# Performance work log

Hardware: AMD Instinct MI355X
Metric: run time of the kernel (lower is better)

## Reference

```python
import jax, jax.numpy as jnp
import numpy as np

C = 256
NUM_HEADS = 8
FFN_HIDDEN = C * 2  # ffn_expand=2
EPS = 1e-5


def setup_inputs() -> dict:
    key = jax.random.key(0)
    ks = jax.random.split(key, 12)
    B, H, W = 16, 64, 64
    s = 0.02
    return {
        "optical": jax.random.normal(ks[0], (B, C, H, W), jnp.float32),
        "sar": jax.random.normal(ks[1], (B, C, H, W), jnp.float32),
        "g_opt": jnp.ones((C,), jnp.float32),
        "b_opt": jnp.zeros((C,), jnp.float32),
        "g_sar": jnp.ones((C,), jnp.float32),
        "b_sar": jnp.zeros((C,), jnp.float32),
        "Wq": jax.random.normal(ks[2], (C, C), jnp.float32) * s,
        "Wk": jax.random.normal(ks[3], (C, C), jnp.float32) * s,
        "Wv": jax.random.normal(ks[4], (C, C), jnp.float32) * s,
        "Wo": jax.random.normal(ks[5], (C, C), jnp.float32) * s,
        "g_ffn": jnp.ones((C,), jnp.float32),
        "b_ffn": jnp.zeros((C,), jnp.float32),
        "W1": jax.random.normal(ks[6], (2 * FFN_HIDDEN, C), jnp.float32) * s,
        "b1": jnp.zeros((2 * FFN_HIDDEN,), jnp.float32),
        "W2": jax.random.normal(ks[7], (C, FFN_HIDDEN), jnp.float32) * s,
        "b2": jnp.zeros((C,), jnp.float32),
    }


def _ln(x, g, b):
    # LayerNorm over channel axis of (B, C, H, W), biased variance, eps=1e-5
    mu = jnp.mean(x, axis=1, keepdims=True)
    var = jnp.mean(jnp.square(x - mu), axis=1, keepdims=True)
    xn = (x - mu) * jax.lax.rsqrt(var + EPS)
    return xn * g[None, :, None, None] + b[None, :, None, None]


def _proj(x, Wmat):
    # 1x1 conv == channel matmul
    return jnp.einsum('oc,bchw->bohw', Wmat, x)


def reference(optical, sar, g_opt, b_opt, g_sar, b_sar, Wq, Wk, Wv, Wo,
              g_ffn, b_ffn, W1, b1, W2, b2):
    B, Cc, H, W = optical.shape
    hc = Cc // NUM_HEADS
    L = H * W
    scale = hc ** -0.5

    opt_n = _ln(optical, g_opt, b_opt)
    sar_n = _ln(sar, g_sar, b_sar)

    # channel (transposed) attention: contraction over spatial L
    q = _proj(opt_n, Wq).reshape(B, NUM_HEADS, hc, L)
    k = _proj(sar_n, Wk).reshape(B, NUM_HEADS, hc, L)
    v = _proj(sar_n, Wv).reshape(B, NUM_HEADS, hc, L)
    A = jax.nn.softmax(jnp.einsum('bhcl,bhdl->bhcd', q, k) * scale, axis=-1)
    attn = jnp.einsum('bhcd,bhdl->bhcl', A, v).reshape(B, Cc, H, W)
    x = optical + _proj(attn, Wo)

    # SimpleGate FFN
    h = _ln(x, g_ffn, b_ffn)
    h = _proj(h, W1) + b1[None, :, None, None]
    h1, h2 = jnp.split(h, 2, axis=1)
    h = _proj(h1 * h2, W2) + b2[None, :, None, None]
    return x + h
```

## Files before the change

### kernel.cpp

```cpp
#include <hip/hip_runtime.h>
#include <hip/hip_bf16.h>

typedef __bf16 bf16;
typedef __attribute__((ext_vector_type(8))) __bf16 bf16x8;
typedef __attribute__((ext_vector_type(4))) __bf16 bf16x4;
typedef __attribute__((ext_vector_type(4))) float f32x4;
typedef __attribute__((ext_vector_type(16))) float f32x16;

#define LSP 4096
#define CCH 256

__device__ __forceinline__ void gl2lds16(const bf16* g, bf16* l) {
  __builtin_amdgcn_global_load_lds(
      (const __attribute__((address_space(1))) unsigned int*)g,
      (__attribute__((address_space(3))) unsigned int*)l, 16, 0, 0);
}

__device__ __forceinline__ f32x4 mfma16(bf16x8 a, bf16x8 b, f32x4 c) {
  return __builtin_amdgcn_mfma_f32_16x16x32_bf16(a, b, c, 0, 0, 0);
}
__device__ __forceinline__ f32x16 mfma32(bf16x8 a, bf16x8 b, f32x16 c) {
  return __builtin_amdgcn_mfma_f32_32x32x16_bf16(a, b, c, 0, 0, 0);
}

__global__ __launch_bounds__(256) void cvt_w_kernel(
    const float* __restrict__ wq, const float* __restrict__ wk,
    const float* __restrict__ wv, const float* __restrict__ wo,
    const float* __restrict__ w1, const float* __restrict__ w2,
    const float* __restrict__ gff, bf16* __restrict__ out) {
  int e = blockIdx.x * 256 + threadIdx.x;
  if (e < 65536)        { out[e] = (bf16)wq[e]; }
  else if (e < 131072)  { out[e] = (bf16)wk[e - 65536]; }
  else if (e < 196608)  {
    int e2 = e - 131072;
    int och = e2 >> 8, cin = e2 & 255;
    out[131072 + cin * 256 + och] = (bf16)wv[e2];
  }
  else if (e < 262144)  { out[e] = (bf16)wo[e - 196608]; }
  else if (e < 524288)  {
    int e2 = e - 262144;
    int m = e2 >> 8, k = e2 & 255;
    int mp = (m < 512) ? (2 * m) : (2 * (m - 512) + 1);
    out[262144 + mp * 256 + k] = (bf16)(w1[e2] * gff[k]);
  }
  else                  { out[e] = (bf16)w2[e - 524288]; }
}

__global__ __launch_bounds__(256) void w1vec_kernel(
    const float* __restrict__ w1, const float* __restrict__ b1,
    const float* __restrict__ gff, const float* __restrict__ bff,
    float* __restrict__ cvec) {
  int m = blockIdx.x * 256 + threadIdx.x;
  const float* row = w1 + (size_t)m * 256;
  float sb = 0.f, sg = 0.f;
  #pragma unroll 8
  for (int c = 0; c < 256; c += 4) {
    f32x4 w = *(const f32x4*)&row[c];
    f32x4 g = *(const f32x4*)&gff[c];
    f32x4 bb = *(const f32x4*)&bff[c];
    #pragma unroll
    for (int j = 0; j < 4; ++j) { sb += w[j] * bb[j]; sg += w[j] * g[j]; }
  }
  if (m < 512) {
    cvec[m] = sb + b1[m];
    cvec[512 + m] = sg;
  } else {
    cvec[512 + m] = sb + b1[m];
    cvec[1024 + m] = sg;
  }
}

template <int DUAL>
__global__ __launch_bounds__(256) void ln_tile_kernel(
    const float* __restrict__ x, const float* __restrict__ gam,
    const float* __restrict__ bet, bf16* __restrict__ out_cl,
    bf16* __restrict__ out_lc) {
  const int l0 = blockIdx.x * 64;
  const int b  = blockIdx.y;
  const int tid = threadIdx.x;
  __shared__ bf16 Tt[256 * 64];
  __shared__ float red[2][16][64];
  __shared__ float mu_s[64], rs_s[64];

  const float* px = x + (size_t)b * CCH * LSP + l0;
  const int colq = (tid & 15) * 4;
  f32x4 s = {0.f, 0.f, 0.f, 0.f}, q = {0.f, 0.f, 0.f, 0.f};
  #pragma unroll
  for (int it = 0; it < 16; ++it) {
    int c = it * 16 + (tid >> 4);
    f32x4 v = *(const f32x4*)&px[(size_t)c * LSP + colq];
    s += v;
    q += v * v;
    bf16x4 h;
    #pragma unroll
    for (int j = 0; j < 4; ++j) h[j] = (bf16)v[j];
    int colp = colq ^ (((c >> 3) & 7) << 3);
    *(bf16x4*)&Tt[c * 64 + colp] = h;
  }
  #pragma unroll
  for (int j = 0; j < 4; ++j) {
    red[0][tid >> 4][colq + j] = s[j];
    red[1][tid >> 4][colq + j] = q[j];
  }
  __syncthreads();
  if (tid < 64) {
    float S = 0.f, Q = 0.f;
    #pragma unroll
    for (int k = 0; k < 16; ++k) { S += red[0][k][tid]; Q += red[1][k][tid]; }
    float m = S * (1.f / 256.f);
    mu_s[tid] = m;
    rs_s[tid] = rsqrtf(Q * (1.f / 256.f) - m * m + 1e-5f);
  }
  __syncthreads();

  #pragma unroll
  for (int it = 0; it < 8; ++it) {
    int ch = it * 256 + tid;
    int c = ch >> 3, col8 = (ch & 7) * 8;
    int colp = col8 ^ (((c >> 3) & 7) << 3);
    bf16x8 h = *(const bf16x8*)&Tt[c * 64 + colp];
    f32x4 m0 = *(const f32x4*)&mu_s[col8];
    f32x4 m1 = *(const f32x4*)&mu_s[col8 + 4];
    f32x4 r0 = *(const f32x4*)&rs_s[col8];
    f32x4 r1 = *(const f32x4*)&rs_s[col8 + 4];
    float g = gam[c], be = bet[c];
    bf16x8 o;
    #pragma unroll
    for (int j = 0; j < 4; ++j) {
      o[j]     = (bf16)(((float)h[j] - m0[j]) * r0[j] * g + be);
      o[4 + j] = (bf16)(((float)h[4 + j] - m1[j]) * r1[j] * g + be);
    }
    *(bf16x8*)&out_cl[((size_t)b * CCH + c) * LSP + l0 + col8] = o;
  }

  if constexpr (DUAL) {
    #pragma unroll
    for (int it = 0; it < 8; ++it) {
      int ch = it * 256 + tid;
      int l = ch >> 5, cch = ch & 31;
      int c0 = cch * 8;
      int lp = l ^ ((cch & 7) << 3);
      float mu = mu_s[l], rs = rs_s[l];
      f32x4 g0 = *(const f32x4*)&gam[c0];
      f32x4 g1 = *(const f32x4*)&gam[c0 + 4];
      f32x4 b0 = *(const f32x4*)&bet[c0];
      f32x4 b1 = *(const f32x4*)&bet[c0 + 4];
      bf16x8 o;
      #pragma unroll
      for (int j = 0; j < 4; ++j) {
        float h0 = (float)Tt[(c0 + j) * 64 + lp];
        float h1 = (float)Tt[(c0 + 4 + j) * 64 + lp];
        o[j]     = (bf16)((h0 - mu) * rs * g0[j] + b0[j]);
        o[4 + j] = (bf16)((h1 - mu) * rs * g1[j] + b1[j]);
      }
      *(bf16x8*)&out_lc[((size_t)b * LSP + l0 + l) * CCH + c0] = o;
    }
  }
}

__global__ __launch_bounds__(256) void gram_kernel(
    const bf16* __restrict__ sar_cl, const bf16* __restrict__ opt_cl,
    float* __restrict__ part) {
  const int tile = blockIdx.x, chunk = blockIdx.y, b = blockIdx.z;
  const int tid = threadIdx.x, lane = tid & 63, w = tid >> 6;
  const int j0 = (tile >> 1) * 128 + (w >> 1) * 64;
  const int i0 = (tile & 1) * 128 + (w & 1) * 64;
  const int l0 = chunk * 1024;
  const bf16* sj = sar_cl + ((size_t)b * CCH + j0 + (lane & 31)) * LSP + l0;
  const bf16* oi = opt_cl + ((size_t)b * CCH + i0 + (lane & 31)) * LSP + l0;
  f32x16 acc[2][2];
  #pragma unroll
  for (int mt = 0; mt < 2; ++mt)
    #pragma unroll
    for (int nt = 0; nt < 2; ++nt)
      #pragma unroll
      for (int r = 0; r < 16; ++r) acc[mt][nt][r] = 0.f;
  #pragma unroll 4
  for (int ks = 0; ks < 64; ++ks) {
    int lofs = ks * 16 + (lane >> 5) * 8;
    bf16x8 a0 = *(const bf16x8*)&sj[lofs];
    bf16x8 a1 = *(const bf16x8*)&sj[32 * LSP + lofs];
    bf16x8 b0 = *(const bf16x8*)&oi[lofs];
    bf16x8 b1 = *(const bf16x8*)&oi[32 * LSP + lofs];
    acc[0][0] = mfma32(a0, b0, acc[0][0]);
    acc[0][1] = mfma32(a0, b1, acc[0][1]);
    acc[1][0] = mfma32(a1, b0, acc[1][0]);
    acc[1][1] = mfma32(a1, b1, acc[1][1]);
  }
  float* op = part + ((size_t)chunk * 16 + b) * 65536;
  #pragma unroll
  for (int mt = 0; mt < 2; ++mt)
    #pragma unroll
    for (int nt = 0; nt < 2; ++nt)
      #pragma unroll
      for (int r = 0; r < 16; ++r) {
        int row = j0 + mt * 32 + (r & 3) + 8 * (r >> 2) + 4 * (lane >> 5);
        int col = i0 + nt * 32 + (lane & 31);
        op[(size_t)row * 256 + col] = acc[mt][nt][r];
      }
}

__global__ __launch_bounds__(256) void greduce_kernel(
    const float* __restrict__ part, bf16* __restrict__ G2) {
  size_t e = ((size_t)blockIdx.x * 256 + threadIdx.x) * 8;
  float a[8];
  #pragma unroll
  for (int i = 0; i < 8; ++i) a[i] = 0.f;
  #pragma unroll
  for (int ch = 0; ch < 4; ++ch) {
    f32x4 p0 = *(const f32x4*)&part[ch * 1048576ull + e];
    f32x4 p1 = *(const f32x4*)&part[ch * 1048576ull + e + 4];
    #pragma unroll
    for (int i = 0; i < 4; ++i) { a[i] += p0[i]; a[4 + i] += p1[i]; }
  }
  bf16x8 o;
  #pragma unroll
  for (int i = 0; i < 8; ++i) o[i] = (bf16)a[i];
  *(bf16x8*)&G2[e] = o;
}

__global__ __launch_bounds__(256) void fold2_kernel(
    const bf16* __restrict__ G2, const bf16* __restrict__ Wq,
    const bf16* __restrict__ Wk, const bf16* __restrict__ WvT,
    bf16* __restrict__ UT) {
  const int bh = blockIdx.x;
  const int b = bh >> 3, h = bh & 7;
  const int tid = threadIdx.x, lane = tid & 63, w = tid >> 6;
  __shared__ bf16 M1[32 * 256];
  __shared__ float Sp[4][1024];
  __shared__ float S[1024];
  __shared__ bf16 P[1024];

  const bf16* gq = Wq + (size_t)(h * 32) * 256;
  const bf16* g2b = G2 + (size_t)b * 65536;
  #pragma unroll
  for (int mt = 0; mt < 2; ++mt)
    #pragma unroll
    for (int nt = 0; nt < 4; ++nt) {
      f32x4 acc = {0.f, 0.f, 0.f, 0.f};
      #pragma unroll
      for (int ks = 0; ks < 8; ++ks) {
        bf16x8 a = *(const bf16x8*)&gq[(size_t)(mt * 16 + (lane & 15)) * 256 +
                                       ks * 32 + (lane >> 4) * 8];
        bf16x8 bb = *(const bf16x8*)&g2b[
            (size_t)(w * 64 + nt * 16 + (lane & 15)) * 256 + ks * 32 +
            (lane >> 4) * 8];
        acc = mfma16(a, bb, acc);
      }
      #pragma unroll
      for (int r = 0; r < 4; ++r)
        M1[(mt * 16 + (lane >> 4) * 4 + r) * 256 + w * 64 + nt * 16 +
           (lane & 15)] = (bf16)acc[r];
    }
  __syncthreads();

  const bf16* gk = Wk + (size_t)(h * 32) * 256;
  #pragma unroll
  for (int mt = 0; mt < 2; ++mt)
    #pragma unroll
    for (int dt = 0; dt < 2; ++dt) {
      f32x4 acc = {0.f, 0.f, 0.f, 0.f};
      #pragma unroll
      for (int kk = 0; kk < 2; ++kk) {
        bf16x8 a = *(const bf16x8*)&M1[(mt * 16 + (lane & 15)) * 256 + w * 64 +
                                       kk * 32 + (lane >> 4) * 8];
        bf16x8 bb = *(const bf16x8*)&gk[(size_t)(dt * 16 + (lane & 15)) * 256 +
                                        w * 64 + kk * 32 + (lane >> 4) * 8];
        acc = mfma16(a, bb, acc);
      }
      #pragma unroll
      for (int r = 0; r < 4; ++r)
        Sp[w][(mt * 16 + (lane >> 4) * 4 + r) * 32 + dt * 16 + (lane & 15)] =
            acc[r];
    }
  __syncthreads();
  #pragma unroll
  for (int i = 0; i < 4; ++i) {
    int e = tid + 256 * i;
    S[e] = (Sp[0][e] + Sp[1][e] + Sp[2][e] + Sp[3][e]) * 0.17677669529663687f;
  }
  __syncthreads();
  if (tid < 32) {
    float m = -1e30f;
    #pragma unroll
    for (int d = 0; d < 32; ++d) m = fmaxf(m, S[tid * 32 + d]);
    float sum = 0.f;
    float ex[32];
    #pragma unroll
    for (int d = 0; d < 32; ++d) {
      ex[d] = __expf(S[tid * 32 + d] - m);
      sum += ex[d];
    }
    float inv = 1.f / sum;
    #pragma unroll
    for (int d = 0; d < 32; ++d) P[tid * 32 + d] = (bf16)(ex[d] * inv);
  }
  __syncthreads();

  bf16x8 bfrag[2];
  #pragma unroll
  for (int ct = 0; ct < 2; ++ct)
    bfrag[ct] =
        *(const bf16x8*)&P[(ct * 16 + (lane & 15)) * 32 + (lane >> 4) * 8];
  bf16* outb = UT + (size_t)b * 65536 + h * 32;
  #pragma unroll
  for (int t = 0; t < 4; ++t) {
    int cin16 = w * 64 + t * 16;
    bf16x8 afrag = *(const bf16x8*)&WvT[(size_t)(cin16 + (lane & 15)) * 256 +
                                        h * 32 + (lane >> 4) * 8];
    #pragma unroll
    for (int ct = 0; ct < 2; ++ct) {
      f32x4 acc = {0.f, 0.f, 0.f, 0.f};
      acc = mfma16(afrag, bfrag[ct], acc);
      int c = ct * 16 + (lane & 15);
      int cinr = cin16 + (lane >> 4) * 4;
      #pragma unroll
      for (int r = 0; r < 4; ++r)
        outb[(size_t)(cinr + r) * 256 + c] = (bf16)acc[r];
    }
  }
}

__global__ __launch_bounds__(256) void wfold_kernel(
    const bf16* __restrict__ Aw, const bf16* __restrict__ Bx,
    bf16* __restrict__ outp) {
  const int tid = threadIdx.x;
  const int lane = tid & 63;
  const int wave = tid >> 6;
  const int wr = wave >> 1, wc = wave & 1;
  const int l0 = blockIdx.x * 128;
  const int m0 = blockIdx.y * 128;
  const int b  = blockIdx.z;
  constexpr int NB = 4096;
  __shared__ bf16 smem[4 * NB];
  bf16* As = smem;
  bf16* Bs = smem + 2 * NB;
  const bf16* Ag = Aw + (size_t)m0 * 256;
  const bf16* Bg = Bx + ((size_t)b * 256 + l0) * 256;
  auto stage = [&](int buf, int k0) {
    #pragma unroll
    for (int i = 0; i < 2; ++i) {
      int ch = i * 256 + tid;
      int r  = ch >> 2;
      int c8 = (ch & 3) * 8;
      gl2lds16(Ag + (size_t)r * 256 + k0 + c8, As + buf * NB + ch * 8);
      gl2lds16(Bg + (size_t)r * 256 + k0 + c8, Bs + buf * NB + ch * 8);
    }
  };
  f32x4 acc[4][4];
  #pragma unroll
  for (int mi = 0; mi < 4; ++mi)
    #pragma unroll
    for (int ni = 0; ni < 4; ++ni)
      #pragma unroll
      for (int r = 0; r < 4; ++r) acc[mi][ni][r] = 0.f;
  stage(0, 0);
  for (int kt = 0; kt < 8; ++kt) {
    __syncthreads();
    if (kt + 1 < 8) stage((kt + 1) & 1, (kt + 1) * 32);
    const bf16* Ab = As + (kt & 1) * NB;
    const bf16* Bb = Bs + (kt & 1) * NB;
    bf16x8 af[4], bfr[4];
    #pragma unroll
    for (int mi = 0; mi < 4; ++mi)
      af[mi] = *(const bf16x8*)&Ab[(wr * 64 + mi * 16 + (lane & 15)) * 32 +
                                   (lane >> 4) * 8];
    #pragma unroll
    for (int ni = 0; ni < 4; ++ni)
      bfr[ni] = *(const bf16x8*)&Bb[(wc * 64 + ni * 16 + (lane & 15)) * 32 +
                                    (lane >> 4) * 8];
    #pragma unroll
    for (int mi = 0; mi < 4; ++mi)
      #pragma unroll
      for (int ni = 0; ni < 4; ++ni)
        acc[mi][ni] = mfma16(af[mi], bfr[ni], acc[mi][ni]);
  }
  const int mq = m0 + wr * 64 + (lane >> 4) * 4;
  const int lq = l0 + wc * 64 + (lane & 15);
  #pragma unroll
  for (int mi = 0; mi < 4; ++mi)
    #pragma unroll
    for (int ni = 0; ni < 4; ++ni) {
      int l = lq + ni * 16, mb = mq + mi * 16;
      #pragma unroll
      for (int r = 0; r < 4; ++r)
        outp[((size_t)b * 256 + mb + r) * 256 + l] = (bf16)acc[mi][ni][r];
    }
}

__global__ __launch_bounds__(256) void xgemm_stats_kernel(
    const bf16* __restrict__ Wfold, const bf16* __restrict__ sar_lc,
    const float* __restrict__ optical, bf16* __restrict__ xout,
    float* __restrict__ stats) {
  const int tid = threadIdx.x, lane = tid & 63, w = tid >> 6;
  const int l0 = blockIdx.x * 64;
  const int b  = blockIdx.y;
  __shared__ __align__(16) char smem[43520];
  bf16* X = (bf16*)smem;
  float* red = (float*)(smem + 40960);

  const bf16* Ag = Wfold + (size_t)b * 65536;
  const bf16* Bg = sar_lc + ((size_t)b * LSP + l0) * CCH;

  auto stage = [&](int buf, int k0) {
    bf16* As = (bf16*)(smem + buf * 16384);
    bf16* Bs = (bf16*)(smem + 32768 + buf * 4096);
    #pragma unroll
    for (int i = 0; i < 4; ++i) {
      int ch = i * 256 + tid;
      int r = ch >> 2, c8 = (ch & 3) * 8;
      gl2lds16(Ag + (size_t)r * 256 + k0 + c8, &As[ch * 8]);
    }
    {
      int r = tid >> 2, c8 = (tid & 3) * 8;
      gl2lds16(Bg + (size_t)r * 256 + k0 + c8, &Bs[tid * 8]);
    }
  };

  f32x4 acc[4][4];
  #pragma unroll
  for (int mi = 0; mi < 4; ++mi)
    #pragma unroll
    for (int ni = 0; ni < 4; ++ni)
      #pragma unroll
      for (int r = 0; r < 4; ++r) acc[mi][ni][r] = 0.f;

  stage(0, 0);
  for (int kt = 0; kt < 8; ++kt) {
    __syncthreads();
    if (kt < 7) stage((kt + 1) & 1, (kt + 1) * 32);
    const bf16* Ab = (const bf16*)(smem + (kt & 1) * 16384);
    const bf16* Bb = (const bf16*)(smem + 32768 + (kt & 1) * 4096);
    bf16x8 af[4], bfr[4];
    #pragma unroll
    for (int mi = 0; mi < 4; ++mi)
      af[mi] = *(const bf16x8*)&Ab[(w * 64 + mi * 16 + (lane & 15)) * 32 +
                                   (lane >> 4) * 8];
    #pragma unroll
    for (int ni = 0; ni < 4; ++ni)
      bfr[ni] = *(const bf16x8*)&Bb[(ni * 16 + (lane & 15)) * 32 +
                                    (lane >> 4) * 8];
    #pragma unroll
    for (int mi = 0; mi < 4; ++mi)
      #pragma unroll
      for (int ni = 0; ni < 4; ++ni)
        acc[mi][ni] = mfma16(af[mi], bfr[ni], acc[mi][ni]);
  }
  __syncthreads();

  const int cb = w * 64 + (lane >> 4) * 4;
  const int lb = lane & 15;
  float s[4], q[4];
  #pragma unroll
  for (int ni = 0; ni < 4; ++ni) { s[ni] = 0.f; q[ni] = 0.f; }
  #pragma unroll
  for (int mi = 0; mi < 4; ++mi)
    #pragma unroll
    for (int ni = 0; ni < 4; ++ni) {
      int c = cb + mi * 16, ll = lb + ni * 16;
      bf16x4 hx;
      #pragma unroll
      for (int r = 0; r < 4; ++r) {
        float v = acc[mi][ni][r] +
                  optical[((size_t)b * CCH + c + r) * LSP + l0 + ll];
        s[ni] += v; q[ni] += v * v;
        hx[r] = (bf16)v;
      }
      *(bf16x4*)&X[ll * 260 + c] = hx;
    }
  #pragma unroll
  for (int ni = 0; ni < 4; ++ni) {
    s[ni] += __shfl_xor(s[ni], 16);
    s[ni] += __shfl_xor(s[ni], 32);
    q[ni] += __shfl_xor(q[ni], 16);
    q[ni] += __shfl_xor(q[ni], 32);
  }
  if ((lane >> 4) == 0) {
    #pragma unroll
    for (int ni = 0; ni < 4; ++ni) {
      red[(0 * 4 + w) * 64 + ni * 16 + lb] = s[ni];
      red[(4 + w) * 64 + ni * 16 + lb] = q[ni];
    }
  }
  __syncthreads();
  if (tid < 64) {
    float S4 = red[0 * 64 + tid] + red[1 * 64 + tid] + red[2 * 64 + tid] +
               red[3 * 64 + tid];
    float Q4 = red[4 * 64 + tid] + red[5 * 64 + tid] + red[6 * 64 + tid] +
               red[7 * 64 + tid];
    float m = S4 * (1.f / 256.f);
    float rs = rsqrtf(Q4 * (1.f / 256.f) - m * m + 1e-5f);
    float* st = stats + ((size_t)b * LSP + l0 + tid) * 2;
    st[0] = m;
    st[1] = rs;
  }
  __syncthreads();
  #pragma unroll
  for (int it = 0; it < 8; ++it) {
    int cid = it * 256 + tid;
    int l = cid >> 5, c0 = (cid & 31) * 8;
    bf16x8 v = *(const bf16x8*)&X[l * 260 + c0];
    *(bf16x8*)&xout[((size_t)b * LSP + l0 + l) * CCH + c0] = v;
  }
}

template <int KEL, int MODE>
__global__ __launch_bounds__(512, 2) void ffn_gemm_kernel(
    const bf16* __restrict__ Aw, const bf16* __restrict__ Bx,
    void* __restrict__ outp, const bf16* __restrict__ resb,
    const float* __restrict__ bias, const float* __restrict__ stats) {
  constexpr int LDSB = (MODE == 1) ? 135168 : 131072;
  __shared__ __align__(16) char smem_raw[LDSB];
  const int tid = threadIdx.x;
  const int lane = tid & 63;
  const int wave = tid >> 6;
  const int wr = wave >> 2;
  const int wc = wave & 3;
  const int l0 = blockIdx.x * 256;
  const int m0 = blockIdx.y * 256;
  const int b  = blockIdx.z;

  char* ldsA0 = smem_raw;
  char* ldsB0 = smem_raw + 32768;
  char* ldsA1 = smem_raw + 65536;
  char* ldsB1 = smem_raw + 98304;

  const bf16* Ag = Aw + (size_t)m0 * KEL;
  const bf16* Bg = Bx + ((size_t)b * LSP + l0) * KEL;

  auto STAGE = [&](const bf16* gsrc, char* ldst, int par, int kt) {
    #pragma unroll
    for (int i = 0; i < 2; ++i) {
      int qi = i * 512 + tid;
      int r  = ((qi >> 7) << 5) + (par << 4) + ((qi >> 3) & 15);
      int cl = (qi & 7) ^ ((qi >> 3) & 7);
      int p  = ((qi >> 7) << 8) + (par << 7) + (qi & 127);
      gl2lds16(gsrc + (size_t)r * KEL + kt * 64 + cl * 8,
               (bf16*)(ldst + p * 16));
    }
  };

  f32x4 acc[8][4];
  #pragma unroll
  for (int mi = 0; mi < 8; ++mi)
    #pragma unroll
    for (int ni = 0; ni < 4; ++ni)
      #pragma unroll
      for (int r = 0; r < 4; ++r) acc[mi][ni][r] = 0.f;

  bf16x8 af[4][2], bf[2][2];
  const int col0 = (((lane >> 4) << 4)) ^ ((lane & 7) << 4);
  const int col1 = col0 ^ 64;
  const int arow_off = (lane & 15) * 128;

#define LOAD_FRAGS(BUFA, BUFB, MP, NP)                                        \
  {                                                                           \
    const char* Ab_ = (BUFA);                                                 \
    const char* Bb_ = (BUFB);                                                 \
    _Pragma("unroll") for (int j = 0; j < 4; ++j) {                           \
      int rb = (wr * 128 + ((MP) + 2 * j) * 16) * 128 + arow_off;             \
      af[j][0] = *(const bf16x8*)(Ab_ + rb + col0);                           \
      af[j][1] = *(const bf16x8*)(Ab_ + rb + col1);                           \
    }                                                                         \
    _Pragma("unroll") for (int i = 0; i < 2; ++i) {                           \
      int rb = (wc * 64 + ((NP) + 2 * i) * 16) * 128 + arow_off;              \
      bf[i][0] = *(const bf16x8*)(Bb_ + rb + col0);                           \
      bf[i][1] = *(const bf16x8*)(Bb_ + rb + col1);                           \
    }                                                                         \
  }

#define DO_MFMA(MP, NP)                                                       \
  _Pragma("unroll") for (int j = 0; j < 4; ++j)                               \
  _Pragma("unroll") for (int i = 0; i < 2; ++i) {                             \
    acc[(MP) + 2 * j][(NP) + 2 * i] =                                         \
        mfma16(af[j][0], bf[i][0], acc[(MP) + 2 * j][(NP) + 2 * i]);          \
    acc[(MP) + 2 * j][(NP) + 2 * i] =                                         \
        mfma16(af[j][1], bf[i][1], acc[(MP) + 2 * j][(NP) + 2 * i]);          \
  }

#define PHASE(BUFA, BUFB, MP, NP, STG)                                        \
  asm volatile("s_waitcnt vmcnt(6)" ::: "memory");                            \
  __builtin_amdgcn_s_barrier();                                               \
  __builtin_amdgcn_sched_barrier(0);                                          \
  LOAD_FRAGS(BUFA, BUFB, MP, NP);                                             \
  STG;                                                                        \
  asm volatile("s_waitcnt lgkmcnt(0)" ::: "memory");                          \
  __builtin_amdgcn_sched_barrier(0);                                          \
  __builtin_amdgcn_s_setprio(1);                                              \
  DO_MFMA(MP, NP);                                                            \
  __builtin_amdgcn_s_setprio(0);

  STAGE(Ag, ldsA0, 0, 0);
  STAGE(Ag, ldsA0, 1, 0);
  STAGE(Bg, ldsB0, 0, 0);
  STAGE(Bg, ldsB0, 1, 0);
  STAGE(Ag, ldsA1, 0, 1);
  STAGE(Bg, ldsB1, 0, 1);

  constexpr int NITER = KEL / 128;
  for (int t = 0; t < NITER; ++t) {
    const int kt1 = 2 * t + 1;
    PHASE(ldsA0, ldsB0, 0, 0, STAGE(Ag, ldsA1, 1, kt1));
    PHASE(ldsA0, ldsB0, 0, 1, STAGE(Bg, ldsB1, 1, kt1));
    PHASE(ldsA0, ldsB0, 1, 0, STAGE(Ag, ldsA0, 0, kt1 + 1));
    PHASE(ldsA0, ldsB0, 1, 1, STAGE(Bg, ldsB0, 0, kt1 + 1));
    PHASE(ldsA1, ldsB1, 0, 0, STAGE(Ag, ldsA0, 1, kt1 + 1));
    PHASE(ldsA1, ldsB1, 0, 1, STAGE(Bg, ldsB0, 1, kt1 + 1));
    PHASE(ldsA1, ldsB1, 1, 0, STAGE(Ag, ldsA1, 0, kt1 + 2));
    PHASE(ldsA1, ldsB1, 1, 1, STAGE(Bg, ldsB1, 0, kt1 + 2));
  }
#undef PHASE
#undef DO_MFMA
#undef LOAD_FRAGS

  asm volatile("s_waitcnt vmcnt(0)" ::: "memory");
  __syncthreads();

  if constexpr (MODE == 0) {
    bf16* g_lds = (bf16*)smem_raw;
    const int lq = wc * 64 + (lane & 15);
    const int qq = (lane >> 4);
    const float* stb = stats + ((size_t)b * LSP + l0) * 2;
    float muv[4], rsv[4];
    #pragma unroll
    for (int ni = 0; ni < 4; ++ni) {
      int l = lq + ni * 16;
      muv[ni] = stb[l * 2];
      rsv[ni] = stb[l * 2 + 1];
    }
    #pragma unroll
    for (int mi = 0; mi < 8; ++mi) {
      int a0 = wr * 64 + mi * 8 + qq * 2;
      int ag = (m0 >> 1) + a0;
      float be1a = bias[ag],        ga1a = bias[512 + ag];
      float be2a = bias[1024 + ag], ga2a = bias[1536 + ag];
      float be1b = bias[ag + 1],        ga1b = bias[512 + ag + 1];
      float be2b = bias[1024 + ag + 1], ga2b = bias[1536 + ag + 1];
      #pragma unroll
      for (int ni = 0; ni < 4; ++ni) {
        int l = lq + ni * 16;
        float mrs = muv[ni] * rsv[ni];
        float h1a = rsv[ni] * acc[mi][ni][0] + be1a - mrs * ga1a;
        float h2a = rsv[ni] * acc[mi][ni][1] + be2a - mrs * ga2a;
        float h1b = rsv[ni] * acc[mi][ni][2] + be1b - mrs * ga1b;
        float h2b = rsv[ni] * acc[mi][ni][3] + be2b - mrs * ga2b;
        bf16 gv0 = (bf16)(h1a * h2a), gv1 = (bf16)(h1b * h2b);
        unsigned u = ((unsigned)*(unsigned short*)&gv1 << 16) |
                     (unsigned)*(unsigned short*)&gv0;
        *(unsigned*)&g_lds[l * 136 + a0] = u;
      }
    }
    __syncthreads();
    bf16* out = (bf16*)outp;
    const int gy = blockIdx.y * 128;
    #pragma unroll
    for (int it = 0; it < 8; ++it) {
      int cid = it * 512 + tid;
      int l = cid >> 4, ch = cid & 15;
      bf16x8 v = *(const bf16x8*)&g_lds[l * 136 + ch * 8];
      *(bf16x8*)&out[((size_t)b * LSP + l0 + l) * 512 + gy + ch * 8] = v;
    }
  } else {
    float* lds_f = (float*)smem_raw;
    float* out = (float*)outp;
    const int lq = wc * 64 + (lane & 15);
    const int qq = (lane >> 4);
    #pragma unroll
    for (int round = 0; round < 2; ++round) {
      if (wr == round) {
        #pragma unroll
        for (int mi = 0; mi < 8; ++mi) {
          int c0 = mi * 16 + qq * 4;
          f32x4 b4 = *(const f32x4*)&bias[round * 128 + c0];
          #pragma unroll
          for (int ni = 0; ni < 4; ++ni) {
            int l = lq + ni * 16;
            bf16x4 xr4 = *(const bf16x4*)&resb[((size_t)b * LSP + l0 + l) *
                                                   CCH + round * 128 + c0];
            #pragma unroll
            for (int r = 0; r < 4; ++r)
              lds_f[(c0 + r) * 260 + l] =
                  acc[mi][ni][r] + b4[r] + (float)xr4[r];
          }
        }
      }
      __syncthreads();
      #pragma unroll
      for (int it = 0; it < 16; ++it) {
        int cid = it * 512 + tid;
        int c = cid >> 6, lch = cid & 63;
        f32x4 v = *(const f32x4*)&lds_f[c * 260 + lch * 4];
        *(f32x4*)&out[((size_t)b * CCH + round * 128 + c) * LSP + l0 +
                      lch * 4] = v;
      }
      __syncthreads();
    }
  }
}

extern "C" void kernel_launch(void* const* d_in, const int* in_sizes, int n_in,
                              void* d_out, int out_size, void* d_ws,
                              size_t ws_size, hipStream_t stream) {
  const float* optical = (const float*)d_in[0];
  const float* sar     = (const float*)d_in[1];
  const float* g_opt   = (const float*)d_in[2];
  const float* b_opt   = (const float*)d_in[3];
  const float* g_sar   = (const float*)d_in[4];
  const float* b_sar   = (const float*)d_in[5];
  const float* Wq      = (const float*)d_in[6];
  const float* Wk      = (const float*)d_in[7];
  const float* Wv      = (const float*)d_in[8];
  const float* Wo      = (const float*)d_in[9];
  const float* g_ffn   = (const float*)d_in[10];
  const float* b_ffn   = (const float*)d_in[11];
  const float* W1      = (const float*)d_in[12];
  const float* b1      = (const float*)d_in[13];
  const float* W2      = (const float*)d_in[14];
  const float* b2      = (const float*)d_in[15];

  char* ws = (char*)d_ws;
  bf16* wbf  = (bf16*)ws;
  bf16* Wqb  = wbf;
  bf16* Wkb  = wbf + 65536;
  bf16* WvTb = wbf + 131072;
  bf16* Wob  = wbf + 196608;
  bf16* W1b  = wbf + 262144;
  bf16* W2b  = wbf + 524288;

  size_t off = 2ull * 1024 * 1024;
  const size_t T16 = 16ull * LSP * CCH * 2;
  bf16* opt_ncl = (bf16*)(ws + off); off += T16;
  bf16* sar_ncl = (bf16*)(ws + off); off += T16;
  bf16* sar_nlc = (bf16*)(ws + off); off += T16;
  bf16* xb      = (bf16*)(ws + off); off += T16;
  float* stats  = (float*)(ws + off); off += 1ull * 1024 * 1024;
  float* cvec   = (float*)(ws + off); off += 64 * 1024;
  float* Gpart  = (float*)(ws + off); off += 16ull * 1024 * 1024;
  bf16* G2b     = (bf16*)(ws + off); off += 4ull * 1024 * 1024;
  bf16* UTb     = (bf16*)(ws + off); off += 2ull * 1024 * 1024;
  bf16* Wfoldb  = (bf16*)(ws + off); off += 2ull * 1024 * 1024;
  bf16* gbuf = opt_ncl;

  dim3 blk(256);
  cvt_w_kernel<<<2560, blk, 0, stream>>>(Wq, Wk, Wv, Wo, W1, W2, g_ffn, wbf);
  w1vec_kernel<<<4, blk, 0, stream>>>(W1, b1, g_ffn, b_ffn, cvec);
  ln_tile_kernel<0><<<dim3(64, 16), blk, 0, stream>>>(optical, g_opt, b_opt,
                                                      opt_ncl, nullptr);
  ln_tile_kernel<1><<<dim3(64, 16), blk, 0, stream>>>(sar, g_sar, b_sar,
                                                      sar_ncl, sar_nlc);
  gram_kernel<<<dim3(4, 4, 16), blk, 0, stream>>>(sar_ncl, opt_ncl, Gpart);
  greduce_kernel<<<512, blk, 0, stream>>>(Gpart, G2b);
  fold2_kernel<<<128, blk, 0, stream>>>(G2b, Wqb, Wkb, WvTb, UTb);
  wfold_kernel<<<dim3(2, 2, 16), blk, 0, stream>>>(Wob, UTb, Wfoldb);
  xgemm_stats_kernel<<<dim3(64, 16), blk, 0, stream>>>(Wfoldb, sar_nlc,
                                                       optical, xb, stats);
  ffn_gemm_kernel<256, 0><<<dim3(16, 4, 16), dim3(512), 0, stream>>>(
      W1b, xb, gbuf, nullptr, cvec, stats);
  ffn_gemm_kernel<512, 1><<<dim3(16, 1, 16), dim3(512), 0, stream>>>(
      W2b, gbuf, (float*)d_out, xb, b2, nullptr);
}
```

Measured before the change: 259.6 us.

## Reuse A/B register fragments across GEMM phases with serpentine order

Splits fragment loading into separate A and B loads and keeps two B fragment sets in registers. The phases now walk the quadrants in a snake order (00, 01, 11, 10), so each phase reloads only A or only B from LDS, cutting LDS read traffic. Global-to-LDS staging is reordered to match, and the k-tile index is clamped at the end. The extra fragment registers raise register pressure, and the new staging order adds risk of hazards between LDS buffer reuse and the waitcnt accounting.

```diff
diff --git a/kernel.cpp b/kernel.cpp
--- a/kernel.cpp
+++ b/kernel.cpp
@@ -548,70 +548,89 @@
       #pragma unroll
       for (int r = 0; r < 4; ++r) acc[mi][ni][r] = 0.f;
 
-  bf16x8 af[4][2], bf[2][2];
+  bf16x8 af[4][2], bn0[2][2], bn1[2][2];
   const int col0 = (((lane >> 4) << 4)) ^ ((lane & 7) << 4);
   const int col1 = col0 ^ 64;
   const int arow_off = (lane & 15) * 128;
 
-#define LOAD_FRAGS(BUFA, BUFB, MP, NP)                                        \
+#define LOAD_A(BUFA, MP)                                                      \
   {                                                                           \
     const char* Ab_ = (BUFA);                                                 \
-    const char* Bb_ = (BUFB);                                                 \
     _Pragma("unroll") for (int j = 0; j < 4; ++j) {                           \
       int rb = (wr * 128 + ((MP) + 2 * j) * 16) * 128 + arow_off;             \
       af[j][0] = *(const bf16x8*)(Ab_ + rb + col0);                           \
       af[j][1] = *(const bf16x8*)(Ab_ + rb + col1);                           \
     }                                                                         \
+  }
+
+#define LOAD_B(BUFB, NP, DST)                                                 \
+  {                                                                           \
+    const char* Bb_ = (BUFB);                                                 \
     _Pragma("unroll") for (int i = 0; i < 2; ++i) {                           \
       int rb = (wc * 64 + ((NP) + 2 * i) * 16) * 128 + arow_off;              \
-      bf[i][0] = *(const bf16x8*)(Bb_ + rb + col0);                           \
-      bf[i][1] = *(const bf16x8*)(Bb_ + rb + col1);                           \
+      DST[i][0] = *(const bf16x8*)(Bb_ + rb + col0);                          \
+      DST[i][1] = *(const bf16x8*)(Bb_ + rb + col1);                          \
     }                                                                         \
   }
 
-#define DO_MFMA(MP, NP)                                                       \
+#define DO_MFMA(MP, NP, BS)                                                   \
   _Pragma("unroll") for (int j = 0; j < 4; ++j)                               \
   _Pragma("unroll") for (int i = 0; i < 2; ++i) {                             \
     acc[(MP) + 2 * j][(NP) + 2 * i] =                                         \
-        mfma16(af[j][0], bf[i][0], acc[(MP) + 2 * j][(NP) + 2 * i]);          \
+        mfma16(af[j][0], BS[i][0], acc[(MP) + 2 * j][(NP) + 2 * i]);          \
     acc[(MP) + 2 * j][(NP) + 2 * i] =                                         \
-        mfma16(af[j][1], bf[i][1], acc[(MP) + 2 * j][(NP) + 2 * i]);          \
-  }
-
-#define PHASE(BUFA, BUFB, MP, NP, STG)                                        \
+        mfma16(af[j][1], BS[i][1], acc[(MP) + 2 * j][(NP) + 2 * i]);          \
+  }
+
+#define PH_HEAD                                                               \
   asm volatile("s_waitcnt vmcnt(6)" ::: "memory");                            \
   __builtin_amdgcn_s_barrier();                                               \
-  __builtin_amdgcn_sched_barrier(0);                                          \
-  LOAD_FRAGS(BUFA, BUFB, MP, NP);                                             \
-  STG;                                                                        \
+  __builtin_amdgcn_sched_barrier(0);
+
+#define PH_TAIL(MP, NP, BS)                                                   \
   asm volatile("s_waitcnt lgkmcnt(0)" ::: "memory");                          \
-  __builtin_amdgcn_sched_barrier(0);                                          \
+  __builtin_amdgcn_sched_barrier(0);                                         \
   __builtin_amdgcn_s_setprio(1);                                              \
-  DO_MFMA(MP, NP);                                                            \
+  DO_MFMA(MP, NP, BS);                                                        \
   __builtin_amdgcn_s_setprio(0);
 
   STAGE(Ag, ldsA0, 0, 0);
-  STAGE(Ag, ldsA0, 1, 0);
   STAGE(Bg, ldsB0, 0, 0);
   STAGE(Bg, ldsB0, 1, 0);
+  STAGE(Ag, ldsA0, 1, 0);
   STAGE(Ag, ldsA1, 0, 1);
-  STAGE(Bg, ldsB1, 0, 1);
+  STAGE(Bg, ldsB1, 1, 1);
 
   constexpr int NITER = KEL / 128;
+  constexpr int KMAX = KEL / 64 - 1;
   for (int t = 0; t < NITER; ++t) {
-    const int kt1 = 2 * t + 1;
-    PHASE(ldsA0, ldsB0, 0, 0, STAGE(Ag, ldsA1, 1, kt1));
-    PHASE(ldsA0, ldsB0, 0, 1, STAGE(Bg, ldsB1, 1, kt1));
-    PHASE(ldsA0, ldsB0, 1, 0, STAGE(Ag, ldsA0, 0, kt1 + 1));
-    PHASE(ldsA0, ldsB0, 1, 1, STAGE(Bg, ldsB0, 0, kt1 + 1));
-    PHASE(ldsA1, ldsB1, 0, 0, STAGE(Ag, ldsA0, 1, kt1 + 1));
-    PHASE(ldsA1, ldsB1, 0, 1, STAGE(Bg, ldsB0, 1, kt1 + 1));
-    PHASE(ldsA1, ldsB1, 1, 0, STAGE(Ag, ldsA1, 0, kt1 + 2));
-    PHASE(ldsA1, ldsB1, 1, 1, STAGE(Bg, ldsB1, 0, kt1 + 2));
-  }
-#undef PHASE
+    const int k1 = 2 * t + 1;
+    const int k2 = (2 * t + 2 > KMAX) ? KMAX : 2 * t + 2;
+    const int k3 = (2 * t + 3 > KMAX) ? KMAX : 2 * t + 3;
+    PH_HEAD; LOAD_A(ldsA0, 0); LOAD_B(ldsB0, 0, bn0);
+    STAGE(Bg, ldsB1, 0, k1); STAGE(Ag, ldsA1, 1, k1);
+    PH_TAIL(0, 0, bn0);
+    PH_HEAD; LOAD_B(ldsB0, 1, bn1);
+    PH_TAIL(0, 1, bn1);
+    PH_HEAD; LOAD_A(ldsA0, 1); STAGE(Ag, ldsA0, 0, k2);
+    PH_TAIL(1, 1, bn1);
+    PH_HEAD; STAGE(Bg, ldsB0, 1, k2);
+    PH_TAIL(1, 0, bn0);
+    PH_HEAD; LOAD_A(ldsA1, 0); LOAD_B(ldsB1, 0, bn0);
+    STAGE(Bg, ldsB0, 0, k2);
+    PH_TAIL(0, 0, bn0);
+    PH_HEAD; LOAD_B(ldsB1, 1, bn1); STAGE(Ag, ldsA0, 1, k2);
+    PH_TAIL(0, 1, bn1);
+    PH_HEAD; LOAD_A(ldsA1, 1); STAGE(Ag, ldsA1, 0, k3);
+    PH_TAIL(1, 1, bn1);
+    PH_HEAD; STAGE(Bg, ldsB1, 1, k3);
+    PH_TAIL(1, 0, bn0);
+  }
+#undef PH_HEAD
+#undef PH_TAIL
 #undef DO_MFMA
-#undef LOAD_FRAGS
+#undef LOAD_A
+#undef LOAD_B
 
   asm volatile("s_waitcnt vmcnt(0)" ::: "memory");
   __syncthreads();
```

Result: no change. 255.0 us (-1.8%).

## Shrink FFN GEMM tiles to 256x128 with simple K=32 double buffering

Applied to the files above, without the earlier changes.

Rewrites the FFN GEMM kernels to use 256x128 output tiles and a simple two-buffer K=32 loop, replacing the hand-scheduled 8-phase pipeline that used 128KB of LDS. LDS drops to 48KB and launch bounds allow 4 blocks per CU, which doubles the grid and raises occupancy. In exchange it gives up the explicit waitcnt/setprio scheduling and the larger tile's data reuse, and adds a barrier per K=32 step. The epilogues are adjusted to the smaller tile, with the MODE 1 output transpose now done in four rounds.

```diff
diff --git a/kernel.cpp b/kernel.cpp
--- a/kernel.cpp
+++ b/kernel.cpp
@@ -505,125 +505,86 @@
 }
 
 template <int KEL, int MODE>
-__global__ __launch_bounds__(512, 2) void ffn_gemm_kernel(
+__global__ __launch_bounds__(512, 4) void ffn_gemm_kernel(
     const bf16* __restrict__ Aw, const bf16* __restrict__ Bx,
     void* __restrict__ outp, const bf16* __restrict__ resb,
     const float* __restrict__ bias, const float* __restrict__ stats) {
-  constexpr int LDSB = (MODE == 1) ? 135168 : 131072;
-  __shared__ __align__(16) char smem_raw[LDSB];
+  __shared__ __align__(16) char smem[49152];
   const int tid = threadIdx.x;
   const int lane = tid & 63;
   const int wave = tid >> 6;
   const int wr = wave >> 2;
   const int wc = wave & 3;
-  const int l0 = blockIdx.x * 256;
+  const int l0 = blockIdx.x * 128;
   const int m0 = blockIdx.y * 256;
   const int b  = blockIdx.z;
 
-  char* ldsA0 = smem_raw;
-  char* ldsB0 = smem_raw + 32768;
-  char* ldsA1 = smem_raw + 65536;
-  char* ldsB1 = smem_raw + 98304;
-
   const bf16* Ag = Aw + (size_t)m0 * KEL;
   const bf16* Bg = Bx + ((size_t)b * LSP + l0) * KEL;
 
-  auto STAGE = [&](const bf16* gsrc, char* ldst, int par, int kt) {
+  auto stage = [&](int buf, int kt) {
+    char* la = smem + (buf << 14);
+    char* lb2 = smem + 32768 + (buf << 13);
     #pragma unroll
     for (int i = 0; i < 2; ++i) {
       int qi = i * 512 + tid;
-      int r  = ((qi >> 7) << 5) + (par << 4) + ((qi >> 3) & 15);
-      int cl = (qi & 7) ^ ((qi >> 3) & 7);
-      int p  = ((qi >> 7) << 8) + (par << 7) + (qi & 127);
-      gl2lds16(gsrc + (size_t)r * KEL + kt * 64 + cl * 8,
-               (bf16*)(ldst + p * 16));
+      int r = qi >> 2, c = qi & 3;
+      int gc = c ^ ((r >> 1) & 3);
+      gl2lds16(Ag + (size_t)r * KEL + kt * 32 + gc * 8,
+               (bf16*)(la + qi * 16));
+    }
+    {
+      int r = tid >> 2, c = tid & 3;
+      int gc = c ^ ((r >> 1) & 3);
+      gl2lds16(Bg + (size_t)r * KEL + kt * 32 + gc * 8,
+               (bf16*)(lb2 + tid * 16));
     }
   };
 
-  f32x4 acc[8][4];
+  f32x4 acc[8][2];
   #pragma unroll
   for (int mi = 0; mi < 8; ++mi)
     #pragma unroll
-    for (int ni = 0; ni < 4; ++ni)
+    for (int ni = 0; ni < 2; ++ni)
       #pragma unroll
       for (int r = 0; r < 4; ++r) acc[mi][ni][r] = 0.f;
 
-  bf16x8 af[4][2], bf[2][2];
-  const int col0 = (((lane >> 4) << 4)) ^ ((lane & 7) << 4);
-  const int col1 = col0 ^ 64;
-  const int arow_off = (lane & 15) * 128;
-
-#define LOAD_FRAGS(BUFA, BUFB, MP, NP)                                        \
-  {                                                                           \
-    const char* Ab_ = (BUFA);                                                 \
-    const char* Bb_ = (BUFB);                                                 \
-    _Pragma("unroll") for (int j = 0; j < 4; ++j) {                           \
-      int rb = (wr * 128 + ((MP) + 2 * j) * 16) * 128 + arow_off;             \
-      af[j][0] = *(const bf16x8*)(Ab_ + rb + col0);                           \
-      af[j][1] = *(const bf16x8*)(Ab_ + rb + col1);                           \
-    }                                                                         \
-    _Pragma("unroll") for (int i = 0; i < 2; ++i) {                           \
-      int rb = (wc * 64 + ((NP) + 2 * i) * 16) * 128 + arow_off;              \
-      bf[i][0] = *(const bf16x8*)(Bb_ + rb + col0);                           \
-      bf[i][1] = *(const bf16x8*)(Bb_ + rb + col1);                           \
-    }                                                                         \
-  }
-
-#define DO_MFMA(MP, NP)                                                       \
-  _Pragma("unroll") for (int j = 0; j < 4; ++j)                               \
-  _Pragma("unroll") for (int i = 0; i < 2; ++i) {                             \
-    acc[(MP) + 2 * j][(NP) + 2 * i] =                                         \
-        mfma16(af[j][0], bf[i][0], acc[(MP) + 2 * j][(NP) + 2 * i]);          \
-    acc[(MP) + 2 * j][(NP) + 2 * i] =                                         \
-        mfma16(af[j][1], bf[i][1], acc[(MP) + 2 * j][(NP) + 2 * i]);          \
-  }
-
-#define PHASE(BUFA, BUFB, MP, NP, STG)                                        \
-  asm volatile("s_waitcnt vmcnt(6)" ::: "memory");                            \
-  __builtin_amdgcn_s_barrier();                                               \
-  __builtin_amdgcn_sched_barrier(0);                                          \
-  LOAD_FRAGS(BUFA, BUFB, MP, NP);                                             \
-  STG;                                                                        \
-  asm volatile("s_waitcnt lgkmcnt(0)" ::: "memory");                          \
-  __builtin_amdgcn_sched_barrier(0);                                          \
-  __builtin_amdgcn_s_setprio(1);                                              \
-  DO_MFMA(MP, NP);                                                            \
-  __builtin_amdgcn_s_setprio(0);
-
-  STAGE(Ag, ldsA0, 0, 0);
-  STAGE(Ag, ldsA0, 1, 0);
-  STAGE(Bg, ldsB0, 0, 0);
-  STAGE(Bg, ldsB0, 1, 0);
-  STAGE(Ag, ldsA1, 0, 1);
-  STAGE(Bg, ldsB1, 0, 1);
-
-  constexpr int NITER = KEL / 128;
-  for (int t = 0; t < NITER; ++t) {
-    const int kt1 = 2 * t + 1;
-    PHASE(ldsA0, ldsB0, 0, 0, STAGE(Ag, ldsA1, 1, kt1));
-    PHASE(ldsA0, ldsB0, 0, 1, STAGE(Bg, ldsB1, 1, kt1));
-    PHASE(ldsA0, ldsB0, 1, 0, STAGE(Ag, ldsA0, 0, kt1 + 1));
-    PHASE(ldsA0, ldsB0, 1, 1, STAGE(Bg, ldsB0, 0, kt1 + 1));
-    PHASE(ldsA1, ldsB1, 0, 0, STAGE(Ag, ldsA0, 1, kt1 + 1));
-    PHASE(ldsA1, ldsB1, 0, 1, STAGE(Bg, ldsB0, 1, kt1 + 1));
-    PHASE(ldsA1, ldsB1, 1, 0, STAGE(Ag, ldsA1, 0, kt1 + 2));
-    PHASE(ldsA1, ldsB1, 1, 1, STAGE(Bg, ldsB1, 0, kt1 + 2));
-  }
-#undef PHASE
-#undef DO_MFMA
-#undef LOAD_FRAGS
-
-  asm volatile("s_waitcnt vmcnt(0)" ::: "memory");
-  __syncthreads();
-
+  constexpr int NK = KEL / 32;
+  stage(0, 0);
+  for (int kt = 0; kt < NK; ++kt) {
+    __syncthreads();
+    if (kt + 1 < NK) stage((kt + 1) & 1, kt + 1);
+    const char* Ab = smem + ((kt & 1) << 14);
+    const char* Bb = smem + 32768 + ((kt & 1) << 13);
+    bf16x8 af[8], bf2[2];
+    #pragma unroll
+    for (int mi = 0; mi < 8; ++mi) {
+      int row = wr * 128 + mi * 16 + (lane & 15);
+      int c = (lane >> 4) ^ ((row >> 1) & 3);
+      af[mi] = *(const bf16x8*)(Ab + row * 64 + c * 16);
+    }
+    #pragma unroll
+    for (int ni = 0; ni < 2; ++ni) {
+      int row = wc * 32 + ni * 16 + (lane & 15);
+      int c = (lane >> 4) ^ ((row >> 1) & 3);
+      bf2[ni] = *(const bf16x8*)(Bb + row * 64 + c * 16);
+    }
+    #pragma unroll
+    for (int mi = 0; mi < 8; ++mi)
+      #pragma unroll
+      for (int ni = 0; ni < 2; ++ni)
+        acc[mi][ni] = mfma16(af[mi], bf2[ni], acc[mi][ni]);
+  }
+  __syncthreads();
+
+  const int qq = lane >> 4;
   if constexpr (MODE == 0) {
-    bf16* g_lds = (bf16*)smem_raw;
-    const int lq = wc * 64 + (lane & 15);
-    const int qq = (lane >> 4);
+    bf16* g_lds = (bf16*)smem;
+    const int lq = wc * 32 + (lane & 15);
     const float* stb = stats + ((size_t)b * LSP + l0) * 2;
-    float muv[4], rsv[4];
-    #pragma unroll
-    for (int ni = 0; ni < 4; ++ni) {
+    float muv[2], rsv[2];
+    #pragma unroll
+    for (int ni = 0; ni < 2; ++ni) {
       int l = lq + ni * 16;
       muv[ni] = stb[l * 2];
       rsv[ni] = stb[l * 2 + 1];
@@ -637,7 +598,7 @@
       float be1b = bias[ag + 1],        ga1b = bias[512 + ag + 1];
       float be2b = bias[1024 + ag + 1], ga2b = bias[1536 + ag + 1];
       #pragma unroll
-      for (int ni = 0; ni < 4; ++ni) {
+      for (int ni = 0; ni < 2; ++ni) {
         int l = lq + ni * 16;
         float mrs = muv[ni] * rsv[ni];
         float h1a = rsv[ni] * acc[mi][ni][0] + be1a - mrs * ga1a;
@@ -654,43 +615,44 @@
     bf16* out = (bf16*)outp;
     const int gy = blockIdx.y * 128;
     #pragma unroll
-    for (int it = 0; it < 8; ++it) {
+    for (int it = 0; it < 4; ++it) {
       int cid = it * 512 + tid;
       int l = cid >> 4, ch = cid & 15;
       bf16x8 v = *(const bf16x8*)&g_lds[l * 136 + ch * 8];
       *(bf16x8*)&out[((size_t)b * LSP + l0 + l) * 512 + gy + ch * 8] = v;
     }
   } else {
-    float* lds_f = (float*)smem_raw;
+    float* lds_f = (float*)smem;
     float* out = (float*)outp;
-    const int lq = wc * 64 + (lane & 15);
-    const int qq = (lane >> 4);
-    #pragma unroll
-    for (int round = 0; round < 2; ++round) {
-      if (wr == round) {
+    const int lq = wc * 32 + (lane & 15);
+    #pragma unroll
+    for (int round = 0; round < 4; ++round) {
+      if (wr == (round >> 1)) {
         #pragma unroll
-        for (int mi = 0; mi < 8; ++mi) {
-          int c0 = mi * 16 + qq * 4;
-          f32x4 b4 = *(const f32x4*)&bias[round * 128 + c0];
+        for (int mj = 0; mj < 4; ++mj) {
+          int mi = (round & 1) * 4 + mj;
+          int c0r = mj * 16 + qq * 4;
+          int cg = round * 64 + c0r;
+          f32x4 b4 = *(const f32x4*)&bias[cg];
           #pragma unroll
-          for (int ni = 0; ni < 4; ++ni) {
+          for (int ni = 0; ni < 2; ++ni) {
             int l = lq + ni * 16;
             bf16x4 xr4 = *(const bf16x4*)&resb[((size_t)b * LSP + l0 + l) *
-                                                   CCH + round * 128 + c0];
+                                                   CCH + cg];
             #pragma unroll
             for (int r = 0; r < 4; ++r)
-              lds_f[(c0 + r) * 260 + l] =
+              lds_f[(c0r + r) * 132 + l] =
                   acc[mi][ni][r] + b4[r] + (float)xr4[r];
           }
         }
       }
       __syncthreads();
       #pragma unroll
-      for (int it = 0; it < 16; ++it) {
+      for (int it = 0; it < 4; ++it) {
         int cid = it * 512 + tid;
-        int c = cid >> 6, lch = cid & 63;
-        f32x4 v = *(const f32x4*)&lds_f[c * 260 + lch * 4];
-        *(f32x4*)&out[((size_t)b * CCH + round * 128 + c) * LSP + l0 +
+        int c = cid >> 5, lch = cid & 31;
+        f32x4 v = *(const f32x4*)&lds_f[c * 132 + lch * 4];
+        *(f32x4*)&out[((size_t)b * CCH + round * 64 + c) * LSP + l0 +
                       lch * 4] = v;
       }
       __syncthreads();
@@ -754,8 +716,8 @@
   wfold_kernel<<<dim3(2, 2, 16), blk, 0, stream>>>(Wob, UTb, Wfoldb);
   xgemm_stats_kernel<<<dim3(64, 16), blk, 0, stream>>>(Wfoldb, sar_nlc,
                                                        optical, xb, stats);
-  ffn_gemm_kernel<256, 0><<<dim3(16, 4, 16), dim3(512), 0, stream>>>(
+  ffn_gemm_kernel<256, 0><<<dim3(32, 4, 16), dim3(512), 0, stream>>>(
       W1b, xb, gbuf, nullptr, cvec, stats);
-  ffn_gemm_kernel<512, 1><<<dim3(16, 1, 16), dim3(512), 0, stream>>>(
+  ffn_gemm_kernel<512, 1><<<dim3(32, 1, 16), dim3(512), 0, stream>>>(
       W2b, gbuf, (float*)d_out, xb, b2, nullptr);
 }
```

Result: no change. 259.5 us (-0.0%).
